# Performance work log

Measured on AMD Instinct MI355X. Metric: run time of the kernel, lower is better.

## Reference

```python
import jax, jax.numpy as jnp
import numpy as np

DIM = 768
H = 12
HD = DIM // H  # 64
B = 16
N = 1025  # cls token + 1024 patches; RoPE applied to tokens 1:


def setup_inputs() -> dict:
    key = jax.random.key(0)
    k1, k2, k3, k4, k5, k6 = jax.random.split(key, 6)
    x = jax.random.normal(k1, (B, N, DIM), dtype=jnp.float32)
    # rotary angles for the N-1 non-cls tokens, HD//2 freq pairs
    theta = jax.random.uniform(k2, (N - 1, HD // 2), dtype=jnp.float32) * 2.0 * jnp.pi
    freqs_cos = jnp.cos(theta)
    freqs_sin = jnp.sin(theta)
    W_qkv = jax.random.normal(k3, (3 * DIM, DIM), dtype=jnp.float32) * 0.02
    W_proj = jax.random.normal(k4, (DIM, DIM), dtype=jnp.float32) * 0.02
    b_proj = jax.random.normal(k5, (DIM,), dtype=jnp.float32) * 0.02
    return {"x": x, "freqs_cos": freqs_cos, "freqs_sin": freqs_sin,
            "W_qkv": W_qkv, "W_proj": W_proj, "b_proj": b_proj}


def _apply_rope(t, cos, sin):
    # t: [b, h, m, d]; cos/sin: [m, d/2]. Pairs are interleaved (even, odd),
    # matching torch.view_as_complex on a (..., d/2, 2) reshape.
    tr = t[..., 0::2]
    ti = t[..., 1::2]
    cos = cos[None, None, :, :]
    sin = sin[None, None, :, :]
    out_r = tr * cos - ti * sin
    out_i = tr * sin + ti * cos
    # interleave back: (..., d/2, 2) -> (..., d)
    out = jnp.stack([out_r, out_i], axis=-1)
    return out.reshape(t.shape)


def reference(x, freqs_cos, freqs_sin, W_qkv, W_proj, b_proj):
    b, n, dim = x.shape
    h, hd = H, HD
    scale = hd ** -0.5

    qkv = jnp.einsum('bnd,ed->bne', x, W_qkv)            # [b, n, 3*dim]
    qkv = qkv.reshape(b, n, 3, h, hd)
    q = jnp.transpose(qkv[:, :, 0], (0, 2, 1, 3))         # [b, h, n, hd]
    k = jnp.transpose(qkv[:, :, 1], (0, 2, 1, 3))
    v = jnp.transpose(qkv[:, :, 2], (0, 2, 1, 3))

    # RoPE on all tokens except the cls token (index 0)
    q = jnp.concatenate([q[:, :, :1], _apply_rope(q[:, :, 1:], freqs_cos, freqs_sin)], axis=2)
    k = jnp.concatenate([k[:, :, :1], _apply_rope(k[:, :, 1:], freqs_cos, freqs_sin)], axis=2)

    dots = jnp.einsum('bhid,bhjd->bhij', q, k) * scale    # [b, h, n, n]
    attn = jax.nn.softmax(dots, axis=-1)
    out = jnp.einsum('bhij,bhjd->bhid', attn, v)          # [b, h, n, hd]
    out = jnp.transpose(out, (0, 2, 1, 3)).reshape(b, n, dim)
    out = jnp.einsum('bnd,ed->bne', out, W_proj) + b_proj
    return out
```

## Files before the change

### kernel.cpp

```cpp
#include <hip/hip_runtime.h>
#include <stdint.h>

#define NH 12
#define HD64 64
#define SEQ 1025
#define M_ROWS (16 * SEQ)
#define DIM 768
#define NPAD 1088

typedef __attribute__((ext_vector_type(8))) short bf16x8;
typedef __attribute__((ext_vector_type(4))) float f32x4;
typedef __attribute__((ext_vector_type(4))) short s16x4;

__device__ __forceinline__ short f2bf_rne(float f) {
    union { float f; uint32_t u; } c; c.f = f;
    uint32_t u = c.u + 0x7fffu + ((c.u >> 16) & 1u);
    return (short)(u >> 16);
}

__device__ __forceinline__ int cvt_pk_bf16(float lo, float hi) {
    int r;
    asm("v_cvt_pk_bf16_f32 %0, %1, %2" : "=v"(r) : "v"(lo), "v"(hi));
    return r;
}

__device__ __forceinline__ void gload_lds16(const void* g, void* l) {
    __builtin_amdgcn_global_load_lds(
        (const __attribute__((address_space(1))) void*)g,
        (__attribute__((address_space(3))) void*)l, 16, 0, 0);
}

__device__ __forceinline__ int xcd_chunk_swizzle(int orig, int nwg) {
    int q = nwg >> 3, r = nwg & 7;
    int xcd = orig & 7, i = orig >> 3;
    int start = (xcd < r) ? xcd * (q + 1) : r * (q + 1) + (xcd - r) * q;
    return start + i;
}

__global__ void f2bf_kernel(const float* __restrict__ in, short* __restrict__ out, int n4) {
    int i = blockIdx.x * blockDim.x + threadIdx.x;
    if (i < n4) {
        f32x4 f = ((const f32x4*)in)[i];
        s16x4 o;
        o[0] = f2bf_rne(f[0]); o[1] = f2bf_rne(f[1]);
        o[2] = f2bf_rne(f[2]); o[3] = f2bf_rne(f[3]);
        ((s16x4*)out)[i] = o;
    }
}

__global__ __launch_bounds__(256) void qkv_gemm_kernel(
    const short* __restrict__ xb, const short* __restrict__ wb,
    const float* __restrict__ fcos, const float* __restrict__ fsin,
    short* __restrict__ Qb, short* __restrict__ Kb, short* __restrict__ VTb)
{
    __shared__ short Alds[2][128 * 32];
    __shared__ short Blds[2][128 * 32];
    const int tid = threadIdx.x;
    const int lane = tid & 63, w = tid >> 6;
    const int wm = w >> 1, wn = w & 1;
    const int lr = lane & 15, lg = lane >> 4;
    const int tile = xcd_chunk_swizzle(blockIdx.x, 129 * 18);
    const int mt = tile / 18, nt = tile - (tile / 18) * 18;

    f32x4 acc[4][4];
#pragma unroll
    for (int i = 0; i < 4; i++)
#pragma unroll
        for (int j = 0; j < 4; j++) acc[i][j] = (f32x4)0.0f;

    auto stage = [&](int buf, int kt) {
#pragma unroll
        for (int i = 0; i < 2; i++) {
            int c = i * 256 + tid;
            int row = c >> 2, cc = c & 3;
            int gr = mt * 128 + row; if (gr > M_ROWS - 1) gr = M_ROWS - 1;
            gload_lds16(xb + (size_t)gr * DIM + kt * 32 + cc * 8, &Alds[buf][c * 8]);
            int gb = nt * 128 + row;
            gload_lds16(wb + (size_t)gb * DIM + kt * 32 + cc * 8, &Blds[buf][c * 8]);
        }
    };

    stage(0, 0);
    asm volatile("s_waitcnt vmcnt(0)" ::: "memory");
    __syncthreads();

    for (int kt = 0; kt < 24; ++kt) {
        int cur = kt & 1;
        if (kt < 23) stage(cur ^ 1, kt + 1);

        bf16x8 af[4], bfr[4];
#pragma unroll
        for (int mi = 0; mi < 4; mi++)
            af[mi] = *(const bf16x8*)&Alds[cur][(wm * 64 + mi * 16 + lr) * 32 + lg * 8];
#pragma unroll
        for (int ni = 0; ni < 4; ni++)
            bfr[ni] = *(const bf16x8*)&Blds[cur][(wn * 64 + ni * 16 + lr) * 32 + lg * 8];
#pragma unroll
        for (int mi = 0; mi < 4; mi++)
#pragma unroll
            for (int ni = 0; ni < 4; ni++)
                acc[mi][ni] = __builtin_amdgcn_mfma_f32_16x16x32_bf16(af[mi], bfr[ni], acc[mi][ni], 0, 0, 0);

        asm volatile("s_waitcnt vmcnt(0)" ::: "memory");
        __syncthreads();
    }

#pragma unroll
    for (int mi = 0; mi < 4; mi++) {
        int mbase = mt * 128 + wm * 64 + mi * 16 + lg * 4;
#pragma unroll
        for (int j = 0; j < 4; j++) {
            int m = mbase + j;
            bool valid = (m < M_ROWS);
            int mm = valid ? m : 0;
            int b = mm / SEQ;
            int n = mm - b * SEQ;
#pragma unroll
            for (int ni = 0; ni < 4; ni++) {
                int e = nt * 128 + wn * 64 + ni * 16 + lr;
                int qkv = e / DIM;
                int rem = e - qkv * DIM;
                int h = rem >> 6, d = rem & 63;
                float v = acc[mi][ni][j];
                float vo = __shfl_xor(v, 1);
                float outv = v;
                if (qkv < 2 && n > 0) {
                    float cs = fcos[(n - 1) * 32 + (d >> 1)];
                    float sn = fsin[(n - 1) * 32 + (d >> 1)];
                    outv = (d & 1) ? (vo * sn + v * cs) : (v * cs - vo * sn);
                }
                if (qkv == 0) outv *= 0.180336881f;
                if (valid) {
                    short bv = f2bf_rne(outv);
                    size_t bh = (size_t)b * NH + h;
                    if (qkv == 0)      Qb[(bh * SEQ + n) * HD64 + d] = bv;
                    else if (qkv == 1) Kb[(bh * SEQ + n) * HD64 + d] = bv;
                    else               VTb[(bh * HD64 + d) * NPAD + n] = bv;
                }
            }
        }
    }
}

__global__ __launch_bounds__(256) void attn_kernel(
    const short* __restrict__ Qb, const short* __restrict__ Kb,
    const short* __restrict__ VTb, short* __restrict__ AO)
{
    __shared__ short Klds[2][64 * 64];
    __shared__ short Vlds[2][64 * 64];
    __shared__ int Plds[4][16 * 32];
    const int tid = threadIdx.x;
    const int lane = tid & 63, w = tid >> 6;
    const int lr = lane & 15, lg = lane >> 4;
    const int tile = xcd_chunk_swizzle(blockIdx.x, 17 * 192);
    const int bh = tile / 17, qt = tile - (tile / 17) * 17;
    const int b = bh / NH, h = bh - b * NH;

    const short* Qp = Qb + (size_t)bh * SEQ * HD64;
    const short* Kp = Kb + (size_t)bh * SEQ * HD64;
    const short* Vp = VTb + (size_t)bh * HD64 * NPAD;

    int qr = qt * 64 + w * 16 + lr; if (qr > SEQ - 1) qr = SEQ - 1;
    bf16x8 qf0 = *(const bf16x8*)&Qp[(size_t)qr * HD64 + 0 + lg * 8];
    bf16x8 qf1 = *(const bf16x8*)&Qp[(size_t)qr * HD64 + 32 + lg * 8];

    float m_i = -1e30f, l_i = 0.f;
    f32x4 acc[4];
#pragma unroll
    for (int vt = 0; vt < 4; vt++) acc[vt] = (f32x4)0.0f;

    int* pw = &Plds[w][0];
    const int pswz = (lr & 3) << 3;

    auto stageKV = [&](int buf, int t) {
        int k0 = t * 64;
#pragma unroll
        for (int i = 0; i < 2; i++) {
            int c = i * 256 + tid;
            int row = c >> 3, ccd = c & 7;
            int cl = ccd ^ (row & 7);
            int krow = k0 + row; if (krow > SEQ - 1) krow = SEQ - 1;
            gload_lds16(Kp + (size_t)krow * HD64 + cl * 8, &Klds[buf][c * 8]);
            gload_lds16(Vp + (size_t)row * NPAD + k0 + cl * 8, &Vlds[buf][c * 8]);
        }
    };

    stageKV(0, 0);
    asm volatile("s_waitcnt vmcnt(0)" ::: "memory");
    __syncthreads();

    for (int t = 0; t < 17; ++t) {
        int cur = t & 1;
        if (t < 16) stageKV(cur ^ 1, t + 1);

        f32x4 s[4];
#pragma unroll
        for (int k16 = 0; k16 < 4; k16++) {
            int krow = k16 * 16 + lr;
            bf16x8 kf0 = *(const bf16x8*)&Klds[cur][krow * 64 + ((0 + lg) ^ (krow & 7)) * 8];
            bf16x8 kf1 = *(const bf16x8*)&Klds[cur][krow * 64 + ((4 + lg) ^ (krow & 7)) * 8];
            f32x4 d = (f32x4)0.0f;
            d = __builtin_amdgcn_mfma_f32_16x16x32_bf16(kf0, qf0, d, 0, 0, 0);
            d = __builtin_amdgcn_mfma_f32_16x16x32_bf16(kf1, qf1, d, 0, 0, 0);
            s[k16] = d;
        }
        if (t == 16) {
            s[0][0] = (lg == 0) ? s[0][0] : -1e30f;
            s[0][1] = -1e30f; s[0][2] = -1e30f; s[0][3] = -1e30f;
#pragma unroll
            for (int k16 = 1; k16 < 4; k16++) { s[k16][0] = -1e30f; s[k16][1] = -1e30f; s[k16][2] = -1e30f; s[k16][3] = -1e30f; }
        }

        float a0 = fmaxf(s[0][0], s[0][1]), a1 = fmaxf(s[0][2], s[0][3]);
        float a2 = fmaxf(s[1][0], s[1][1]), a3 = fmaxf(s[1][2], s[1][3]);
        float a4 = fmaxf(s[2][0], s[2][1]), a5 = fmaxf(s[2][2], s[2][3]);
        float a6 = fmaxf(s[3][0], s[3][1]), a7 = fmaxf(s[3][2], s[3][3]);
        float b0 = fmaxf(fmaxf(a0, a1), fmaxf(a2, a3));
        float b1 = fmaxf(fmaxf(a4, a5), fmaxf(a6, a7));
        float pmax = fmaxf(b0, b1);
        pmax = fmaxf(pmax, __shfl_xor(pmax, 16));
        pmax = fmaxf(pmax, __shfl_xor(pmax, 32));

        if (__any(pmax > m_i + 11.54f)) {
            float mnew = fmaxf(m_i, pmax);
            float sc = exp2f(m_i - mnew);
            m_i = mnew;
            l_i *= sc;
#pragma unroll
            for (int j = 0; j < 4; j++) {
                float scj = __shfl(sc, 4 * lg + j);
#pragma unroll
                for (int vt = 0; vt < 4; vt++) acc[vt][j] *= scj;
            }
        }

#pragma unroll
        for (int k16 = 0; k16 < 4; k16++) {
#pragma unroll
            for (int j = 0; j < 4; j++) s[k16][j] = exp2f(s[k16][j] - m_i);
        }
        float r0 = (s[0][0] + s[0][1]) + (s[0][2] + s[0][3]);
        float r1 = (s[1][0] + s[1][1]) + (s[1][2] + s[1][3]);
        float r2 = (s[2][0] + s[2][1]) + (s[2][2] + s[2][3]);
        float r3 = (s[3][0] + s[3][1]) + (s[3][2] + s[3][3]);
        float rowsum = (r0 + r1) + (r2 + r3);
        rowsum += __shfl_xor(rowsum, 16);
        rowsum += __shfl_xor(rowsum, 32);
        l_i += rowsum;

#pragma unroll
        for (int k16 = 0; k16 < 4; k16++) {
            int pk0 = cvt_pk_bf16(s[k16][0], s[k16][1]);
            int pk1 = cvt_pk_bf16(s[k16][2], s[k16][3]);
            int pbase = 8 * k16 + 2 * lg;
            pw[lr * 32 + ((pbase + 0) ^ pswz)] = pk0;
            pw[lr * 32 + ((pbase + 1) ^ pswz)] = pk1;
        }
        bf16x8 pa0 = *(const bf16x8*)&pw[lr * 32 + ((4 * lg) ^ pswz)];
        bf16x8 pa1 = *(const bf16x8*)&pw[lr * 32 + ((16 + 4 * lg) ^ pswz)];

#pragma unroll
        for (int vt = 0; vt < 4; vt++) {
            int dr = vt * 16 + lr;
            bf16x8 vf0 = *(const bf16x8*)&Vlds[cur][dr * 64 + ((0 + lg) ^ (dr & 7)) * 8];
            bf16x8 vf1 = *(const bf16x8*)&Vlds[cur][dr * 64 + ((4 + lg) ^ (dr & 7)) * 8];
            acc[vt] = __builtin_amdgcn_mfma_f32_16x16x32_bf16(pa0, vf0, acc[vt], 0, 0, 0);
            acc[vt] = __builtin_amdgcn_mfma_f32_16x16x32_bf16(pa1, vf1, acc[vt], 0, 0, 0);
        }

        asm volatile("s_waitcnt vmcnt(0)" ::: "memory");
        __syncthreads();
    }

    float inv[4];
#pragma unroll
    for (int j = 0; j < 4; j++) inv[j] = 1.0f / __shfl(l_i, 4 * lg + j);
#pragma unroll
    for (int vt = 0; vt < 4; vt++) {
#pragma unroll
        for (int j = 0; j < 4; j++) {
            int qrow = qt * 64 + w * 16 + lg * 4 + j;
            if (qrow < SEQ) {
                AO[((size_t)(b * SEQ + qrow)) * DIM + h * HD64 + vt * 16 + lr] =
                    f2bf_rne(acc[vt][j] * inv[j]);
            }
        }
    }
}

__global__ __launch_bounds__(256) void proj_gemm_kernel(
    const short* __restrict__ ab, const short* __restrict__ wb,
    const float* __restrict__ bias, float* __restrict__ out)
{
    __shared__ short Alds[2][128 * 32];
    __shared__ short Blds[2][128 * 32];
    const int tid = threadIdx.x;
    const int lane = tid & 63, w = tid >> 6;
    const int wm = w >> 1, wn = w & 1;
    const int lr = lane & 15, lg = lane >> 4;
    const int tile = xcd_chunk_swizzle(blockIdx.x, 129 * 6);
    const int mt = tile / 6, nt = tile - (tile / 6) * 6;

    f32x4 acc[4][4];
#pragma unroll
    for (int i = 0; i < 4; i++)
#pragma unroll
        for (int j = 0; j < 4; j++) acc[i][j] = (f32x4)0.0f;

    auto stage = [&](int buf, int kt) {
#pragma unroll
        for (int i = 0; i < 2; i++) {
            int c = i * 256 + tid;
            int row = c >> 2, cc = c & 3;
            int gr = mt * 128 + row; if (gr > M_ROWS - 1) gr = M_ROWS - 1;
            gload_lds16(ab + (size_t)gr * DIM + kt * 32 + cc * 8, &Alds[buf][c * 8]);
            int gb = nt * 128 + row;
            gload_lds16(wb + (size_t)gb * DIM + kt * 32 + cc * 8, &Blds[buf][c * 8]);
        }
    };

    stage(0, 0);
    asm volatile("s_waitcnt vmcnt(0)" ::: "memory");
    __syncthreads();

    for (int kt = 0; kt < 24; ++kt) {
        int cur = kt & 1;
        if (kt < 23) stage(cur ^ 1, kt + 1);

        bf16x8 af[4], bfr[4];
#pragma unroll
        for (int mi = 0; mi < 4; mi++)
            af[mi] = *(const bf16x8*)&Alds[cur][(wm * 64 + mi * 16 + lr) * 32 + lg * 8];
#pragma unroll
        for (int ni = 0; ni < 4; ni++)
            bfr[ni] = *(const bf16x8*)&Blds[cur][(wn * 64 + ni * 16 + lr) * 32 + lg * 8];
#pragma unroll
        for (int mi = 0; mi < 4; mi++)
#pragma unroll
            for (int ni = 0; ni < 4; ni++)
                acc[mi][ni] = __builtin_amdgcn_mfma_f32_16x16x32_bf16(af[mi], bfr[ni], acc[mi][ni], 0, 0, 0);

        asm volatile("s_waitcnt vmcnt(0)" ::: "memory");
        __syncthreads();
    }

#pragma unroll
    for (int ni = 0; ni < 4; ni++) {
        int e = nt * 128 + wn * 64 + ni * 16 + lr;
        float bv = bias[e];
#pragma unroll
        for (int mi = 0; mi < 4; mi++) {
#pragma unroll
            for (int j = 0; j < 4; j++) {
                int m = mt * 128 + wm * 64 + mi * 16 + lg * 4 + j;
                if (m < M_ROWS) out[(size_t)m * DIM + e] = acc[mi][ni][j] + bv;
            }
        }
    }
}

extern "C" void kernel_launch(void* const* d_in, const int* in_sizes, int n_in,
                              void* d_out, int out_size, void* d_ws, size_t ws_size,
                              hipStream_t stream) {
    const float* x     = (const float*)d_in[0];
    const float* fcos  = (const float*)d_in[1];
    const float* fsin  = (const float*)d_in[2];
    const float* wqkv  = (const float*)d_in[3];
    const float* wproj = (const float*)d_in[4];
    const float* bproj = (const float*)d_in[5];
    float* out = (float*)d_out;

    char* ws = (char*)d_ws;
    size_t off = 0;
    auto salloc = [&](size_t bytes) { void* p = ws + off; off += (bytes + 255) & ~(size_t)255; return p; };
    short* xb     = (short*)salloc((size_t)M_ROWS * DIM * 2);
    short* wqkvb  = (short*)salloc((size_t)2304 * DIM * 2);
    short* wprojb = (short*)salloc((size_t)DIM * DIM * 2);
    short* Qb     = (short*)salloc((size_t)192 * SEQ * HD64 * 2);
    short* Kb     = (short*)salloc((size_t)192 * SEQ * HD64 * 2);
    short* VTb    = (short*)salloc((size_t)192 * HD64 * NPAD * 2);
    short* AO     = (short*)salloc((size_t)M_ROWS * DIM * 2);

    {
        int n4 = M_ROWS * DIM / 4;
        f2bf_kernel<<<(n4 + 255) / 256, 256, 0, stream>>>(x, xb, n4);
    }
    {
        int n4 = 2304 * DIM / 4;
        f2bf_kernel<<<(n4 + 255) / 256, 256, 0, stream>>>(wqkv, wqkvb, n4);
    }
    {
        int n4 = DIM * DIM / 4;
        f2bf_kernel<<<(n4 + 255) / 256, 256, 0, stream>>>(wproj, wprojb, n4);
    }

    qkv_gemm_kernel<<<129 * 18, 256, 0, stream>>>(xb, wqkvb, fcos, fsin, Qb, Kb, VTb);
    attn_kernel<<<17 * 192, 256, 0, stream>>>(Qb, Kb, VTb, AO);
    proj_gemm_kernel<<<129 * 6, 256, 0, stream>>>(AO, wprojb, bproj, out);
}
```

Before: 355.8 us.

## Use triple-buffered LDS pipeline with partial vmcnt waits in QKV and proj GEMMs

```diff
diff --git a/kernel.cpp b/kernel.cpp
--- a/kernel.cpp
+++ b/kernel.cpp
@@ -11,6 +11,9 @@
 typedef __attribute__((ext_vector_type(8))) short bf16x8;
 typedef __attribute__((ext_vector_type(4))) float f32x4;
 typedef __attribute__((ext_vector_type(4))) short s16x4;
+
+#define VMCNT(n) asm volatile("s_waitcnt vmcnt(" #n ")" ::: "memory")
+#define LGKMCNT0 asm volatile("s_waitcnt lgkmcnt(0)" ::: "memory")
 
 __device__ __forceinline__ short f2bf_rne(float f) {
     union { float f; uint32_t u; } c; c.f = f;
@@ -53,8 +56,8 @@
     const float* __restrict__ fcos, const float* __restrict__ fsin,
     short* __restrict__ Qb, short* __restrict__ Kb, short* __restrict__ VTb)
 {
-    __shared__ short Alds[2][128 * 32];
-    __shared__ short Blds[2][128 * 32];
+    __shared__ short Alds[3][128 * 32];
+    __shared__ short Blds[3][128 * 32];
     const int tid = threadIdx.x;
     const int lane = tid & 63, w = tid >> 6;
     const int wm = w >> 1, wn = w & 1;
@@ -62,47 +65,63 @@
     const int tile = xcd_chunk_swizzle(blockIdx.x, 129 * 18);
     const int mt = tile / 18, nt = tile - (tile / 18) * 18;
 
+    const int c0 = tid, c1 = 256 + tid;
+    int ra0 = mt * 128 + (c0 >> 2); if (ra0 > M_ROWS - 1) ra0 = M_ROWS - 1;
+    int ra1 = mt * 128 + (c1 >> 2); if (ra1 > M_ROWS - 1) ra1 = M_ROWS - 1;
+    const short* gA0 = xb + (size_t)ra0 * DIM + (c0 & 3) * 8;
+    const short* gA1 = xb + (size_t)ra1 * DIM + (c1 & 3) * 8;
+    const short* gB0 = wb + (size_t)(nt * 128 + (c0 >> 2)) * DIM + (c0 & 3) * 8;
+    const short* gB1 = wb + (size_t)(nt * 128 + (c1 >> 2)) * DIM + (c1 & 3) * 8;
+    short* lA0 = &Alds[0][0] + c0 * 8;
+    short* lA1 = &Alds[0][0] + c1 * 8;
+    short* lB0 = &Blds[0][0] + c0 * 8;
+    short* lB1 = &Blds[0][0] + c1 * 8;
+
+    auto stage = [&](int buf, int kt) {
+        const int ko = kt * 32;
+        const int lo = buf * (128 * 32);
+        gload_lds16(gA0 + ko, lA0 + lo);
+        gload_lds16(gA1 + ko, lA1 + lo);
+        gload_lds16(gB0 + ko, lB0 + lo);
+        gload_lds16(gB1 + ko, lB1 + lo);
+    };
+
     f32x4 acc[4][4];
 #pragma unroll
     for (int i = 0; i < 4; i++)
 #pragma unroll
         for (int j = 0; j < 4; j++) acc[i][j] = (f32x4)0.0f;
 
-    auto stage = [&](int buf, int kt) {
-#pragma unroll
-        for (int i = 0; i < 2; i++) {
-            int c = i * 256 + tid;
-            int row = c >> 2, cc = c & 3;
-            int gr = mt * 128 + row; if (gr > M_ROWS - 1) gr = M_ROWS - 1;
-            gload_lds16(xb + (size_t)gr * DIM + kt * 32 + cc * 8, &Alds[buf][c * 8]);
-            int gb = nt * 128 + row;
-            gload_lds16(wb + (size_t)gb * DIM + kt * 32 + cc * 8, &Blds[buf][c * 8]);
-        }
-    };
-
-    stage(0, 0);
-    asm volatile("s_waitcnt vmcnt(0)" ::: "memory");
-    __syncthreads();
-
-    for (int kt = 0; kt < 24; ++kt) {
-        int cur = kt & 1;
-        if (kt < 23) stage(cur ^ 1, kt + 1);
+    stage(0, 0); stage(1, 1); stage(2, 2);
+
+    int cur = 0;
+    for (int t = 0; t < 24; ++t) {
+        if (t <= 21) { VMCNT(8); } else if (t == 22) { VMCNT(4); } else { VMCNT(0); }
+        __builtin_amdgcn_s_barrier();
 
         bf16x8 af[4], bfr[4];
+        const short* Ab = &Alds[0][0] + cur * (128 * 32);
+        const short* Bb = &Blds[0][0] + cur * (128 * 32);
 #pragma unroll
         for (int mi = 0; mi < 4; mi++)
-            af[mi] = *(const bf16x8*)&Alds[cur][(wm * 64 + mi * 16 + lr) * 32 + lg * 8];
+            af[mi] = *(const bf16x8*)&Ab[(wm * 64 + mi * 16 + lr) * 32 + lg * 8];
 #pragma unroll
         for (int ni = 0; ni < 4; ni++)
-            bfr[ni] = *(const bf16x8*)&Blds[cur][(wn * 64 + ni * 16 + lr) * 32 + lg * 8];
+            bfr[ni] = *(const bf16x8*)&Bb[(wn * 64 + ni * 16 + lr) * 32 + lg * 8];
+
+        if (t <= 20) {
+            LGKMCNT0;
+            __builtin_amdgcn_s_barrier();
+            stage(cur, t + 3);
+        }
+
 #pragma unroll
         for (int mi = 0; mi < 4; mi++)
 #pragma unroll
             for (int ni = 0; ni < 4; ni++)
                 acc[mi][ni] = __builtin_amdgcn_mfma_f32_16x16x32_bf16(af[mi], bfr[ni], acc[mi][ni], 0, 0, 0);
 
-        asm volatile("s_waitcnt vmcnt(0)" ::: "memory");
-        __syncthreads();
+        cur = (cur == 2) ? 0 : cur + 1;
     }
 
 #pragma unroll
@@ -292,8 +311,8 @@
     const short* __restrict__ ab, const short* __restrict__ wb,
     const float* __restrict__ bias, float* __restrict__ out)
 {
-    __shared__ short Alds[2][128 * 32];
-    __shared__ short Blds[2][128 * 32];
+    __shared__ short Alds[3][128 * 32];
+    __shared__ short Blds[3][128 * 32];
     const int tid = threadIdx.x;
     const int lane = tid & 63, w = tid >> 6;
     const int wm = w >> 1, wn = w & 1;
@@ -301,47 +320,63 @@
     const int tile = xcd_chunk_swizzle(blockIdx.x, 129 * 6);
     const int mt = tile / 6, nt = tile - (tile / 6) * 6;
 
+    const int c0 = tid, c1 = 256 + tid;
+    int ra0 = mt * 128 + (c0 >> 2); if (ra0 > M_ROWS - 1) ra0 = M_ROWS - 1;
+    int ra1 = mt * 128 + (c1 >> 2); if (ra1 > M_ROWS - 1) ra1 = M_ROWS - 1;
+    const short* gA0 = ab + (size_t)ra0 * DIM + (c0 & 3) * 8;
+    const short* gA1 = ab + (size_t)ra1 * DIM + (c1 & 3) * 8;
+    const short* gB0 = wb + (size_t)(nt * 128 + (c0 >> 2)) * DIM + (c0 & 3) * 8;
+    const short* gB1 = wb + (size_t)(nt * 128 + (c1 >> 2)) * DIM + (c1 & 3) * 8;
+    short* lA0 = &Alds[0][0] + c0 * 8;
+    short* lA1 = &Alds[0][0] + c1 * 8;
+    short* lB0 = &Blds[0][0] + c0 * 8;
+    short* lB1 = &Blds[0][0] + c1 * 8;
+
+    auto stage = [&](int buf, int kt) {
+        const int ko = kt * 32;
+        const int lo = buf * (128 * 32);
+        gload_lds16(gA0 + ko, lA0 + lo);
+        gload_lds16(gA1 + ko, lA1 + lo);
+        gload_lds16(gB0 + ko, lB0 + lo);
+        gload_lds16(gB1 + ko, lB1 + lo);
+    };
+
     f32x4 acc[4][4];
 #pragma unroll
     for (int i = 0; i < 4; i++)
 #pragma unroll
         for (int j = 0; j < 4; j++) acc[i][j] = (f32x4)0.0f;
 
-    auto stage = [&](int buf, int kt) {
-#pragma unroll
-        for (int i = 0; i < 2; i++) {
-            int c = i * 256 + tid;
-            int row = c >> 2, cc = c & 3;
-            int gr = mt * 128 + row; if (gr > M_ROWS - 1) gr = M_ROWS - 1;
-            gload_lds16(ab + (size_t)gr * DIM + kt * 32 + cc * 8, &Alds[buf][c * 8]);
-            int gb = nt * 128 + row;
-            gload_lds16(wb + (size_t)gb * DIM + kt * 32 + cc * 8, &Blds[buf][c * 8]);
-        }
-    };
-
-    stage(0, 0);
-    asm volatile("s_waitcnt vmcnt(0)" ::: "memory");
-    __syncthreads();
-
-    for (int kt = 0; kt < 24; ++kt) {
-        int cur = kt & 1;
-        if (kt < 23) stage(cur ^ 1, kt + 1);
+    stage(0, 0); stage(1, 1); stage(2, 2);
+
+    int cur = 0;
+    for (int t = 0; t < 24; ++t) {
+        if (t <= 21) { VMCNT(8); } else if (t == 22) { VMCNT(4); } else { VMCNT(0); }
+        __builtin_amdgcn_s_barrier();
 
         bf16x8 af[4], bfr[4];
+        const short* Ab = &Alds[0][0] + cur * (128 * 32);
+        const short* Bb = &Blds[0][0] + cur * (128 * 32);
 #pragma unroll
         for (int mi = 0; mi < 4; mi++)
-            af[mi] = *(const bf16x8*)&Alds[cur][(wm * 64 + mi * 16 + lr) * 32 + lg * 8];
+            af[mi] = *(const bf16x8*)&Ab[(wm * 64 + mi * 16 + lr) * 32 + lg * 8];
 #pragma unroll
         for (int ni = 0; ni < 4; ni++)
-            bfr[ni] = *(const bf16x8*)&Blds[cur][(wn * 64 + ni * 16 + lr) * 32 + lg * 8];
+            bfr[ni] = *(const bf16x8*)&Bb[(wn * 64 + ni * 16 + lr) * 32 + lg * 8];
+
+        if (t <= 20) {
+            LGKMCNT0;
+            __builtin_amdgcn_s_barrier();
+            stage(cur, t + 3);
+        }
+
 #pragma unroll
         for (int mi = 0; mi < 4; mi++)
 #pragma unroll
             for (int ni = 0; ni < 4; ni++)
                 acc[mi][ni] = __builtin_amdgcn_mfma_f32_16x16x32_bf16(af[mi], bfr[ni], acc[mi][ni], 0, 0, 0);
 
-        asm volatile("s_waitcnt vmcnt(0)" ::: "memory");
-        __syncthreads();
+        cur = (cur == 2) ? 0 : cur + 1;
     }
 
 #pragma unroll
```

Result: faster. 336.4 us (-5.5%).
